# Kernel optimization log

Measured on AMD Instinct MI355X. Metric: run time of the kernel, lower is better.

## Reference

```python
import jax, jax.numpy as jnp
import numpy as np

V = 200000   # vocab_size
P = 50       # pos_size
D = 64       # vocab_dim
DP = 64      # pos_dim
B = 4096
T = 50
S = 64       # num_sampled
MASK_VAL = -2.0 ** 32  # matches deepmatch SoftmaxWeightedSum padding value


def setup_inputs() -> dict:
    key = jax.random.key(0)
    ks = jax.random.split(key, 10)
    items_id = jax.random.randint(ks[0], (B, T), 0, V)
    position_id = jax.random.randint(ks[1], (B, T), 0, P)
    target_id = jax.random.randint(ks[2], (B, 1), 0, V)
    keys_length = jax.random.randint(ks[3], (B, 1), 1, T + 1)  # at least 1 valid key
    sampled_ids = jax.random.randint(ks[4], (S,), 0, V)
    item_table = jax.random.normal(ks[5], (V, D), dtype=jnp.float32) * 0.05
    pos_table = jax.random.normal(ks[6], (P, DP), dtype=jnp.float32) * 0.05
    att_W = jax.random.normal(ks[7], (D + DP, 1), dtype=jnp.float32) * 0.05
    att_b = jnp.zeros((1,), dtype=jnp.float32)
    prelu_alpha = jnp.full((D,), 0.25, dtype=jnp.float32)
    zero_bias = jnp.zeros((V,), dtype=jnp.float32)
    return {
        "item_table": item_table, "pos_table": pos_table, "att_W": att_W,
        "att_b": att_b, "prelu_alpha": prelu_alpha, "zero_bias": zero_bias,
        "items_id": items_id, "position_id": position_id, "target_id": target_id,
        "keys_length": keys_length, "sampled_ids": sampled_ids,
    }


def _log_uniform_logq(ids):
    # log-uniform (Zipf) sampler probability used by tf sampled_softmax_loss
    idf = ids.astype(jnp.float32)
    q = (jnp.log(idf + 2.0) - jnp.log(idf + 1.0)) / jnp.log(float(V + 1))
    return jnp.log(q)


def reference(item_table, pos_table, att_W, att_b, prelu_alpha, zero_bias,
              items_id, position_id, target_id, keys_length, sampled_ids):
    items = item_table[items_id]          # [B,T,D]
    position = pos_table[position_id]     # [B,T,DP]
    target = item_table[target_id]        # [B,1,D]

    # ConcatAttention: tanh(Dense1(concat(items, position)))
    qk = jnp.concatenate([items, position], axis=-1)          # [B,T,D+DP]
    score = jnp.tanh(qk @ att_W + att_b)                       # [B,T,1]

    # SoftmaxWeightedSum: masked softmax over T, elementwise-weighted values
    key_mask = jnp.arange(T)[None, :] < keys_length            # [B,T]
    masked = jnp.where(key_mask[..., None], score, MASK_VAL)   # [B,T,1]
    weights = jax.nn.softmax(masked, axis=1)                   # [B,T,1]
    sum_pooling_before = weights * items                       # [B,T,D]

    sum_pooling = sum_pooling_before.sum(axis=1, keepdims=True)  # [B,1,D]
    # PReLU with per-channel alpha
    sum_pooling = jnp.where(sum_pooling > 0, sum_pooling, prelu_alpha * sum_pooling)

    # output = sum_pooling @ target^T -> [B,1]
    output = jnp.einsum('bud,bvd->buv', sum_pooling, target)[:, 0]  # [B,1]

    # aux_mask=True branch
    padding = (items_id != 0).astype(sum_pooling_before.dtype)[..., None]  # [B,T,1]
    spb = sum_pooling_before * padding
    # get_diff_col: last valid item per row
    result = items_id[jnp.arange(B), keys_length[:, 0] - 1]    # [B]

    ut_1 = spb[:, :-1, :].sum(axis=1)                          # [B,D]

    # sampled softmax loss (determinized: fixed sampled_ids, log-uniform correction)
    true_w = item_table[result]                                # [B,D]
    true_logit = jnp.sum(ut_1 * true_w, axis=-1) + zero_bias[result]      # [B]
    samp_w = item_table[sampled_ids]                           # [S,D]
    samp_logits = ut_1 @ samp_w.T + zero_bias[sampled_ids][None, :]        # [B,S]
    true_logit = true_logit - _log_uniform_logq(result)
    samp_logits = samp_logits - _log_uniform_logq(sampled_ids)[None, :]
    # remove accidental hits
    hit = sampled_ids[None, :] == result[:, None]
    samp_logits = jnp.where(hit, samp_logits - 1e9, samp_logits)
    logits = jnp.concatenate([true_logit[:, None], samp_logits], axis=-1)  # [B,1+S]
    loss = jnp.mean(-jax.nn.log_softmax(logits, axis=-1)[:, 0])

    return (output, loss)
```

## Files before the change

### kernel.cpp

```cpp
#include <hip/hip_runtime.h>
#include <hip/hip_bf16.h>
#include <math.h>

#define Tt 50
#define Dd 64
#define Bb 4096
#define Ss 64
#define ROWP 68

template <int CTRL>
__device__ __forceinline__ float dppperm(float x) {
  return __builtin_bit_cast(
      float, __builtin_amdgcn_update_dpp(0, __builtin_bit_cast(int, x), CTRL,
                                         0xF, 0xF, true));
}
#define DPP_XOR1 0xB1
#define DPP_XOR2 0x4E
#define DPP_XOR7 0x141
#define DPP_XOR15 0x140

__device__ __forceinline__ float gsum16(float v) {
  v += dppperm<DPP_XOR1>(v);
  v += dppperm<DPP_XOR2>(v);
  v += dppperm<DPP_XOR7>(v);
  v += dppperm<DPP_XOR15>(v);
  return v;
}
__device__ __forceinline__ float wsum(float v) {
  v = gsum16(v);
  v += __shfl_xor(v, 16, 64);
  v += __shfl_xor(v, 32, 64);
  return v;
}
__device__ __forceinline__ float wmax(float v) {
  v = fmaxf(v, dppperm<DPP_XOR1>(v));
  v = fmaxf(v, dppperm<DPP_XOR2>(v));
  v = fmaxf(v, dppperm<DPP_XOR7>(v));
  v = fmaxf(v, dppperm<DPP_XOR15>(v));
  v = fmaxf(v, __shfl_xor(v, 16, 64));
  v = fmaxf(v, __shfl_xor(v, 32, 64));
  return v;
}
__device__ __forceinline__ float bf2f(unsigned short u) {
  return __uint_as_float(((unsigned)u) << 16);
}
__device__ __forceinline__ unsigned short f2bf(float f) {
  __hip_bfloat16 h = __float2bfloat16(f);
  return __builtin_bit_cast(unsigned short, h);
}
__device__ __forceinline__ float logq_f(int id) {
  float idf = (float)id;
  float r = log1pf(1.0f / (idf + 1.0f));
  return __logf(r * (1.0f / 12.2060776f));
}
__device__ __forceinline__ float fast_tanh(float x) {
  float ex = __expf(2.0f * x);
  return 1.0f - 2.0f * __builtin_amdgcn_rcpf(ex + 1.0f);
}

__global__ __launch_bounds__(256, 4) void u2i_main(
    const float* __restrict__ item_table,
    const float* __restrict__ pos_table,
    const float* __restrict__ att_W,
    const float* __restrict__ att_b,
    const float* __restrict__ prelu_alpha,
    const float* __restrict__ zero_bias,
    const int* __restrict__ items_id,
    const int* __restrict__ position_id,
    const int* __restrict__ target_id,
    const int* __restrict__ keys_length,
    const int* __restrict__ sampled_ids,
    float* __restrict__ out_vec,
    float* __restrict__ loss_ws)
{
  __shared__ unsigned short sampB[Ss][ROWP];
  __shared__ float ut1_lds[4][Dd];
  __shared__ float red[4];

  const int tid = threadIdx.x;
  const int lane = tid & 63;
  const int w = tid >> 6;
  const int b = (blockIdx.x << 2) | w;
  const int sub = lane >> 4;
  const int dg = lane & 15;
  const int d0g = dg << 2;

  int idreg = 0, pidreg = 0;
  if (lane < Tt) {
    idreg = items_id[b * Tt + lane];
    pidreg = position_id[b * Tt + lane];
  }
  const int kl = keys_length[b];
  const int tgt = target_id[b];
  const int sid = sampled_ids[lane];
  const int result = __shfl(idreg, kl - 1, 64);
  float4 tv4 = *(const float4*)&item_table[(size_t)tgt * Dd + d0g];
  float4 tw4 = *(const float4*)&item_table[(size_t)result * Dd + d0g];
  const float zb_r = zero_bias[result];
  const float zb_s = zero_bias[sid];

#pragma unroll
  for (int k = 0; k < 4; ++k) {
    int s = (tid >> 4) + 16 * k;
    float4 x = *(const float4*)&item_table[(size_t)sampled_ids[s] * Dd + ((tid & 15) << 2)];
    ushort4 o;
    o.x = f2bf(x.x); o.y = f2bf(x.y); o.z = f2bf(x.z); o.w = f2bf(x.w);
    *(ushort4*)&sampB[s][(tid & 15) << 2] = o;
  }
  __syncthreads();

  const float4 Wi4 = *(const float4*)&att_W[d0g];
  const float4 Wp4 = *(const float4*)&att_W[Dd + d0g];
  unsigned pk0[13], pk1[13];
  float v[13];
#pragma unroll
  for (int c = 0; c < 13; ++c) {
    const int t = 4 * c + sub;
    const int tt = (t < Tt) ? t : 0;
    int iid = __shfl(idreg, tt, 64);
    int pid = __shfl(pidreg, tt, 64);
    float4 x = *(const float4*)&item_table[(size_t)iid * Dd + d0g];
    float4 p = *(const float4*)&pos_table[pid * Dd + d0g];
    v[c] = x.x * Wi4.x + x.y * Wi4.y + x.z * Wi4.z + x.w * Wi4.w +
           p.x * Wp4.x + p.y * Wp4.y + p.z * Wp4.z + p.w * Wp4.w;
    pk0[c] = ((unsigned)f2bf(x.y) << 16) | f2bf(x.x);
    pk1[c] = ((unsigned)f2bf(x.w) << 16) | f2bf(x.z);
  }
#pragma unroll
  for (int c = 0; c < 13; ++c) v[c] = gsum16(v[c]);

  const float ab = att_b[0];
  float lmax = -INFINITY;
#pragma unroll
  for (int c = 0; c < 13; ++c) {
    const int t = 4 * c + sub;
    v[c] = fast_tanh(v[c] + ab);
    if (t < kl) lmax = fmaxf(lmax, v[c]);
  }
  lmax = fmaxf(lmax, __shfl_xor(lmax, 16, 64));
  lmax = fmaxf(lmax, __shfl_xor(lmax, 32, 64));
  float lsum = 0.0f;
#pragma unroll
  for (int c = 0; c < 13; ++c) {
    const int t = 4 * c + sub;
    float e = (t < kl) ? __expf(v[c] - lmax) : 0.0f;
    v[c] = e;
    lsum += e;
  }
  lsum += __shfl_xor(lsum, 16, 64);
  lsum += __shfl_xor(lsum, 32, 64);
  const float inv = __builtin_amdgcn_rcpf(lsum);
  const unsigned long long mask = __ballot(lane < Tt - 1 && idreg != 0);

  float4 sp4 = make_float4(0, 0, 0, 0), u14 = make_float4(0, 0, 0, 0);
#pragma unroll
  for (int c = 0; c < 13; ++c) {
    const int t = 4 * c + sub;
    float wt = v[c] * inv;
    float wm = ((mask >> t) & 1ull) ? wt : 0.0f;
    float x0 = bf2f((unsigned short)pk0[c]);
    float x1 = bf2f((unsigned short)(pk0[c] >> 16));
    float x2 = bf2f((unsigned short)pk1[c]);
    float x3 = bf2f((unsigned short)(pk1[c] >> 16));
    sp4.x += wt * x0; sp4.y += wt * x1; sp4.z += wt * x2; sp4.w += wt * x3;
    u14.x += wm * x0; u14.y += wm * x1; u14.z += wm * x2; u14.w += wm * x3;
  }
#pragma unroll
  for (int mm = 16; mm <= 32; mm <<= 1) {
    sp4.x += __shfl_xor(sp4.x, mm, 64); sp4.y += __shfl_xor(sp4.y, mm, 64);
    sp4.z += __shfl_xor(sp4.z, mm, 64); sp4.w += __shfl_xor(sp4.w, mm, 64);
    u14.x += __shfl_xor(u14.x, mm, 64); u14.y += __shfl_xor(u14.y, mm, 64);
    u14.z += __shfl_xor(u14.z, mm, 64); u14.w += __shfl_xor(u14.w, mm, 64);
  }

  float4 al = *(const float4*)&prelu_alpha[d0g];
  float4 sp;
  sp.x = sp4.x > 0.0f ? sp4.x : al.x * sp4.x;
  sp.y = sp4.y > 0.0f ? sp4.y : al.y * sp4.y;
  sp.z = sp4.z > 0.0f ? sp4.z : al.z * sp4.z;
  sp.w = sp4.w > 0.0f ? sp4.w : al.w * sp4.w;
  float op = sp.x * tv4.x + sp.y * tv4.y + sp.z * tv4.z + sp.w * tv4.w;
  float tp = u14.x * tw4.x + u14.y * tw4.y + u14.z * tw4.z + u14.w * tw4.w;
  op = gsum16(op);
  tp = gsum16(tp);
  if (lane == 0) out_vec[b] = op;
  float tl = tp + zb_r - logq_f(result);
  if (lane < 16) *(float4*)&ut1_lds[w][d0g] = u14;

  const ushort4* srow = (const ushort4*)&sampB[lane][0];
  const float4* up = (const float4*)&ut1_lds[w][0];
  float acc = 0.0f;
#pragma unroll
  for (int q = 0; q < 16; ++q) {
    ushort4 u = srow[q];
    float4 uv = up[q];
    acc += bf2f(u.x) * uv.x + bf2f(u.y) * uv.y + bf2f(u.z) * uv.z +
           bf2f(u.w) * uv.w;
  }
  float sl = acc + zb_s - logq_f(sid);
  if (sid == result) sl -= 1e9f;
  float mx = fmaxf(tl, wmax(sl));
  float se = wsum(__expf(sl - mx)) + __expf(tl - mx);
  float loss_b = (mx + __logf(se)) - tl;
  if (lane == 0) red[w] = loss_b;
  __syncthreads();
  if (tid == 0) loss_ws[blockIdx.x] = (red[0] + red[1]) + (red[2] + red[3]);
}

__global__ __launch_bounds__(256) void loss_reduce_kernel(
    const float* __restrict__ ws, float* __restrict__ out_loss) {
  __shared__ float red[4];
  const int tid = threadIdx.x;
  float acc = ws[tid] + ws[tid + 256] + ws[tid + 512] + ws[tid + 768];
  acc = wsum(acc);
  if ((tid & 63) == 0) red[tid >> 6] = acc;
  __syncthreads();
  if (tid == 0)
    out_loss[0] = ((red[0] + red[1]) + (red[2] + red[3])) * (1.0f / (float)Bb);
}

extern "C" void kernel_launch(void* const* d_in, const int* in_sizes, int n_in,
                              void* d_out, int out_size, void* d_ws, size_t ws_size,
                              hipStream_t stream) {
  const float* item_table  = (const float*)d_in[0];
  const float* pos_table   = (const float*)d_in[1];
  const float* att_W       = (const float*)d_in[2];
  const float* att_b       = (const float*)d_in[3];
  const float* prelu_alpha = (const float*)d_in[4];
  const float* zero_bias   = (const float*)d_in[5];
  const int* items_id      = (const int*)d_in[6];
  const int* position_id   = (const int*)d_in[7];
  const int* target_id     = (const int*)d_in[8];
  const int* keys_length   = (const int*)d_in[9];
  const int* sampled_ids   = (const int*)d_in[10];

  float* out = (float*)d_out;
  float* loss_ws = (float*)d_ws;

  u2i_main<<<Bb / 4, 256, 0, stream>>>(
      item_table, pos_table, att_W, att_b, prelu_alpha, zero_bias,
      items_id, position_id, target_id, keys_length, sampled_ids,
      out, loss_ws);
  loss_reduce_kernel<<<1, 256, 0, stream>>>(loss_ws, out + Bb);
}
```

Measured before the change: 20.31 us.

## Split each batch row across two waves by halving the embedding dimension

Each batch row is now handled by two waves, each covering 32 of the 64 embedding dims, so blocks grow to 512 threads. Partial attention scores and the final dot products are exchanged through shared memory, with extra block barriers. Each lane gathers 7 time steps instead of 13, which shortens the per-wave serial gather chain and raises memory-level parallelism. The cost is more synchronisation, half of the waves sitting idle during the sampled-softmax phase, and possibly lower occupancy under launch_bounds(512,4).

```diff
diff --git a/kernel.cpp b/kernel.cpp
--- a/kernel.cpp
+++ b/kernel.cpp
@@ -19,6 +19,12 @@
 #define DPP_XOR7 0x141
 #define DPP_XOR15 0x140
 
+__device__ __forceinline__ float gsum8(float v) {
+  v += dppperm<DPP_XOR1>(v);
+  v += dppperm<DPP_XOR2>(v);
+  v += dppperm<DPP_XOR7>(v);
+  return v;
+}
 __device__ __forceinline__ float gsum16(float v) {
   v += dppperm<DPP_XOR1>(v);
   v += dppperm<DPP_XOR2>(v);
@@ -58,7 +64,7 @@
   return 1.0f - 2.0f * __builtin_amdgcn_rcpf(ex + 1.0f);
 }
 
-__global__ __launch_bounds__(256, 4) void u2i_main(
+__global__ __launch_bounds__(512, 4) void u2i_main(
     const float* __restrict__ item_table,
     const float* __restrict__ pos_table,
     const float* __restrict__ att_W,
@@ -74,16 +80,20 @@
     float* __restrict__ loss_ws)
 {
   __shared__ unsigned short sampB[Ss][ROWP];
+  __shared__ float score_lds[4][2][56];
   __shared__ float ut1_lds[4][Dd];
+  __shared__ float part_lds[4][2][2];
   __shared__ float red[4];
 
   const int tid = threadIdx.x;
   const int lane = tid & 63;
-  const int w = tid >> 6;
-  const int b = (blockIdx.x << 2) | w;
-  const int sub = lane >> 4;
-  const int dg = lane & 15;
-  const int d0g = dg << 2;
+  const int wave = tid >> 6;
+  const int j = wave >> 1;
+  const int half = wave & 1;
+  const int b = (blockIdx.x << 2) | j;
+  const int sub8 = lane >> 3;
+  const int dg8 = lane & 7;
+  const int d0 = half * 32 + (dg8 << 2);
 
   int idreg = 0, pidreg = 0;
   if (lane < Tt) {
@@ -94,59 +104,66 @@
   const int tgt = target_id[b];
   const int sid = sampled_ids[lane];
   const int result = __shfl(idreg, kl - 1, 64);
-  float4 tv4 = *(const float4*)&item_table[(size_t)tgt * Dd + d0g];
-  float4 tw4 = *(const float4*)&item_table[(size_t)result * Dd + d0g];
+  float4 tv4 = *(const float4*)&item_table[(size_t)tgt * Dd + d0];
+  float4 tw4 = *(const float4*)&item_table[(size_t)result * Dd + d0];
   const float zb_r = zero_bias[result];
   const float zb_s = zero_bias[sid];
 
 #pragma unroll
-  for (int k = 0; k < 4; ++k) {
-    int s = (tid >> 4) + 16 * k;
-    float4 x = *(const float4*)&item_table[(size_t)sampled_ids[s] * Dd + ((tid & 15) << 2)];
+  for (int k = 0; k < 2; ++k) {
+    int s = (tid >> 4) + 32 * k;
+    int sd = (tid & 15) << 2;
+    float4 x = *(const float4*)&item_table[(size_t)sampled_ids[s] * Dd + sd];
     ushort4 o;
     o.x = f2bf(x.x); o.y = f2bf(x.y); o.z = f2bf(x.z); o.w = f2bf(x.w);
-    *(ushort4*)&sampB[s][(tid & 15) << 2] = o;
-  }
-  __syncthreads();
-
-  const float4 Wi4 = *(const float4*)&att_W[d0g];
-  const float4 Wp4 = *(const float4*)&att_W[Dd + d0g];
-  unsigned pk0[13], pk1[13];
-  float v[13];
-#pragma unroll
-  for (int c = 0; c < 13; ++c) {
-    const int t = 4 * c + sub;
+    *(ushort4*)&sampB[s][sd] = o;
+  }
+
+  const float4 Wi4 = *(const float4*)&att_W[d0];
+  const float4 Wp4 = *(const float4*)&att_W[Dd + d0];
+  unsigned pk0[7], pk1[7];
+  float v[7];
+#pragma unroll
+  for (int c = 0; c < 7; ++c) {
+    const int t = 8 * c + sub8;
     const int tt = (t < Tt) ? t : 0;
     int iid = __shfl(idreg, tt, 64);
     int pid = __shfl(pidreg, tt, 64);
-    float4 x = *(const float4*)&item_table[(size_t)iid * Dd + d0g];
-    float4 p = *(const float4*)&pos_table[pid * Dd + d0g];
+    float4 x = *(const float4*)&item_table[(size_t)iid * Dd + d0];
+    float4 p = *(const float4*)&pos_table[pid * Dd + d0];
     v[c] = x.x * Wi4.x + x.y * Wi4.y + x.z * Wi4.z + x.w * Wi4.w +
            p.x * Wp4.x + p.y * Wp4.y + p.z * Wp4.z + p.w * Wp4.w;
     pk0[c] = ((unsigned)f2bf(x.y) << 16) | f2bf(x.x);
     pk1[c] = ((unsigned)f2bf(x.w) << 16) | f2bf(x.z);
   }
 #pragma unroll
-  for (int c = 0; c < 13; ++c) v[c] = gsum16(v[c]);
+  for (int c = 0; c < 7; ++c) v[c] = gsum8(v[c]);
+  if (dg8 == 0) {
+#pragma unroll
+    for (int c = 0; c < 7; ++c) score_lds[j][half][8 * c + sub8] = v[c];
+  }
+  __syncthreads();
 
   const float ab = att_b[0];
   float lmax = -INFINITY;
 #pragma unroll
-  for (int c = 0; c < 13; ++c) {
-    const int t = 4 * c + sub;
-    v[c] = fast_tanh(v[c] + ab);
+  for (int c = 0; c < 7; ++c) {
+    const int t = 8 * c + sub8;
+    v[c] = fast_tanh(v[c] + score_lds[j][half ^ 1][t] + ab);
     if (t < kl) lmax = fmaxf(lmax, v[c]);
   }
+  lmax = fmaxf(lmax, __shfl_xor(lmax, 8, 64));
   lmax = fmaxf(lmax, __shfl_xor(lmax, 16, 64));
   lmax = fmaxf(lmax, __shfl_xor(lmax, 32, 64));
   float lsum = 0.0f;
 #pragma unroll
-  for (int c = 0; c < 13; ++c) {
-    const int t = 4 * c + sub;
+  for (int c = 0; c < 7; ++c) {
+    const int t = 8 * c + sub8;
     float e = (t < kl) ? __expf(v[c] - lmax) : 0.0f;
     v[c] = e;
     lsum += e;
   }
+  lsum += __shfl_xor(lsum, 8, 64);
   lsum += __shfl_xor(lsum, 16, 64);
   lsum += __shfl_xor(lsum, 32, 64);
   const float inv = __builtin_amdgcn_rcpf(lsum);
@@ -154,8 +171,8 @@
 
   float4 sp4 = make_float4(0, 0, 0, 0), u14 = make_float4(0, 0, 0, 0);
 #pragma unroll
-  for (int c = 0; c < 13; ++c) {
-    const int t = 4 * c + sub;
+  for (int c = 0; c < 7; ++c) {
+    const int t = 8 * c + sub8;
     float wt = v[c] * inv;
     float wm = ((mask >> t) & 1ull) ? wt : 0.0f;
     float x0 = bf2f((unsigned short)pk0[c]);
@@ -166,14 +183,14 @@
     u14.x += wm * x0; u14.y += wm * x1; u14.z += wm * x2; u14.w += wm * x3;
   }
 #pragma unroll
-  for (int mm = 16; mm <= 32; mm <<= 1) {
+  for (int mm = 8; mm <= 32; mm <<= 1) {
     sp4.x += __shfl_xor(sp4.x, mm, 64); sp4.y += __shfl_xor(sp4.y, mm, 64);
     sp4.z += __shfl_xor(sp4.z, mm, 64); sp4.w += __shfl_xor(sp4.w, mm, 64);
     u14.x += __shfl_xor(u14.x, mm, 64); u14.y += __shfl_xor(u14.y, mm, 64);
     u14.z += __shfl_xor(u14.z, mm, 64); u14.w += __shfl_xor(u14.w, mm, 64);
   }
 
-  float4 al = *(const float4*)&prelu_alpha[d0g];
+  float4 al = *(const float4*)&prelu_alpha[d0];
   float4 sp;
   sp.x = sp4.x > 0.0f ? sp4.x : al.x * sp4.x;
   sp.y = sp4.y > 0.0f ? sp4.y : al.y * sp4.y;
@@ -181,28 +198,36 @@
   sp.w = sp4.w > 0.0f ? sp4.w : al.w * sp4.w;
   float op = sp.x * tv4.x + sp.y * tv4.y + sp.z * tv4.z + sp.w * tv4.w;
   float tp = u14.x * tw4.x + u14.y * tw4.y + u14.z * tw4.z + u14.w * tw4.w;
-  op = gsum16(op);
-  tp = gsum16(tp);
-  if (lane == 0) out_vec[b] = op;
-  float tl = tp + zb_r - logq_f(result);
-  if (lane < 16) *(float4*)&ut1_lds[w][d0g] = u14;
-
-  const ushort4* srow = (const ushort4*)&sampB[lane][0];
-  const float4* up = (const float4*)&ut1_lds[w][0];
-  float acc = 0.0f;
-#pragma unroll
-  for (int q = 0; q < 16; ++q) {
-    ushort4 u = srow[q];
-    float4 uv = up[q];
-    acc += bf2f(u.x) * uv.x + bf2f(u.y) * uv.y + bf2f(u.z) * uv.z +
-           bf2f(u.w) * uv.w;
-  }
-  float sl = acc + zb_s - logq_f(sid);
-  if (sid == result) sl -= 1e9f;
-  float mx = fmaxf(tl, wmax(sl));
-  float se = wsum(__expf(sl - mx)) + __expf(tl - mx);
-  float loss_b = (mx + __logf(se)) - tl;
-  if (lane == 0) red[w] = loss_b;
+  op = gsum8(op);
+  tp = gsum8(tp);
+  if (lane == 0) {
+    part_lds[j][half][0] = op;
+    part_lds[j][half][1] = tp;
+  }
+  if (sub8 == 0) *(float4*)&ut1_lds[j][d0] = u14;
+  __syncthreads();
+
+  if (half == 0) {
+    if (lane == 0) out_vec[b] = part_lds[j][0][0] + part_lds[j][1][0];
+    float tl = part_lds[j][0][1] + part_lds[j][1][1] + zb_r - logq_f(result);
+
+    const ushort4* srow = (const ushort4*)&sampB[lane][0];
+    const float4* up = (const float4*)&ut1_lds[j][0];
+    float acc = 0.0f;
+#pragma unroll
+    for (int q = 0; q < 16; ++q) {
+      ushort4 u = srow[q];
+      float4 uv = up[q];
+      acc += bf2f(u.x) * uv.x + bf2f(u.y) * uv.y + bf2f(u.z) * uv.z +
+             bf2f(u.w) * uv.w;
+    }
+    float sl = acc + zb_s - logq_f(sid);
+    if (sid == result) sl -= 1e9f;
+    float mx = fmaxf(tl, wmax(sl));
+    float se = wsum(__expf(sl - mx)) + __expf(tl - mx);
+    float loss_b = (mx + __logf(se)) - tl;
+    if (lane == 0) red[j] = loss_b;
+  }
   __syncthreads();
   if (tid == 0) loss_ws[blockIdx.x] = (red[0] + red[1]) + (red[2] + red[3]);
 }
@@ -237,7 +262,7 @@
   float* out = (float*)d_out;
   float* loss_ws = (float*)d_ws;
 
-  u2i_main<<<Bb / 4, 256, 0, stream>>>(
+  u2i_main<<<Bb / 4, 512, 0, stream>>>(
       item_table, pos_table, att_W, att_b, prelu_alpha, zero_bias,
       items_id, position_id, target_id, keys_length, sampled_ids,
       out, loss_ws);
```

Result: slower. 24.99 us (+23.0%).
